# Kernel tuning notes

Measured on AMD Instinct MI355X. Metric: run time of the kernel, lower is better.

Reference implementation:

```python
import jax, jax.numpy as jnp
import numpy as np

B, NH, WH, WW, C, NPOS = 64, 16, 16, 16, 64, 288
N = WH * WW


def setup_inputs() -> dict:
    key = jax.random.key(0)
    k1, k2, k3 = jax.random.split(key, 3)
    query = jax.random.normal(k1, (B, NH, N, C), dtype=jnp.float32)
    attn_logits = jax.random.normal(k2, (B, NH, N, N), dtype=jnp.float32)
    pos_emb = jax.random.normal(k3, (C, NPOS), dtype=jnp.float32) * 0.02
    return {"query": query, "attn_logits": attn_logits, "pos_emb": pos_emb,
            "Wh": WH, "Ww": WW, "npos_max": NPOS}


def _rev_cumsum(x):
    # flip -> cumsum -> flip along last axis
    return jnp.flip(jnp.cumsum(jnp.flip(x, -1), axis=-1), -1)


def reference(query, attn_logits, pos_emb, Wh, Ww, npos_max):
    B_, nH, N_, C_ = query.shape
    gates = jax.nn.sigmoid(attn_logits)                       # (B,nH,N,N)
    gates_h = gates.swapaxes(-1, -2).reshape(B_, nH, N_, Ww, Wh)
    gates_w = gates.reshape(B_, nH, N_, Wh, Ww)
    pos_h = _rev_cumsum(gates_h).reshape(B_, nH, N_, N_).swapaxes(-1, -2)
    pos_w = _rev_cumsum(gates_w).reshape(B_, nH, N_, N_)
    pos = pos_h * Ww + pos_w
    pos = jnp.minimum(pos, npos_max - 1)
    pos_floor = jnp.floor(pos)
    pos_ceil_i = jnp.ceil(pos).astype(jnp.int32)
    pos_floor_i = pos_floor.astype(jnp.int32)
    # (B,nH,N,C) @ (C,npos) -> (B,nH,N,npos)
    logits_int = jnp.einsum('bhnc,cp->bhnp', query, pos_emb)
    logits_ceil = jnp.take_along_axis(logits_int, pos_ceil_i, axis=-1)
    logits_floor = jnp.take_along_axis(logits_int, pos_floor_i, axis=-1)
    w = pos - pos_floor
    return logits_ceil * w + logits_floor * (1.0 - w)
```

## Files before the change

### kernel.cpp

```cpp
#include <hip/hip_runtime.h>


#define NPOS 288
#define NT   18
#define LTSF 292

typedef __attribute__((ext_vector_type(8))) short bf16x8;
typedef __attribute__((ext_vector_type(4))) float f32x4;

__device__ __forceinline__ unsigned short f2bf(float f) {
    unsigned u = __float_as_uint(f);
    u += 0x7FFF + ((u >> 16) & 1);
    return (unsigned short)(u >> 16);
}
__device__ __forceinline__ unsigned cvt_pk_bf16(float lo, float hi) {
    unsigned r;
    asm("v_cvt_pk_bf16_f32 %0, %1, %2" : "=v"(r) : "v"(lo), "v"(hi));
    return r;
}
__device__ __forceinline__ float fast_exp2(float x) {
    float r;
    asm("v_exp_f32 %0, %1" : "=v"(r) : "v"(x));
    return r;
}
__device__ __forceinline__ float fast_fract(float x) {
    float r;
    asm("v_fract_f32 %0, %1" : "=v"(r) : "v"(x));
    return r;
}

template <int D>
__device__ __forceinline__ float suffix_step(float v) {
    int s = __builtin_amdgcn_update_dpp(0, __float_as_int(v), 0x100 | D, 0xF, 0xF, true);
    return v + __int_as_float(s);
}

__global__ void prep_kernel(const float* __restrict__ pos_emb,
                            short* __restrict__ wsb) {
    int idx = blockIdx.x * blockDim.x + threadIdx.x;
    if (idx >= NT * 2 * 64) return;
    int l = idx & 63;
    int s = (idx >> 6) & 1;
    int t = idx >> 7;
    int col = t * 16 + (l & 15);
    int k0  = s * 32 + (l >> 4) * 8;
    short* dst = wsb + idx * 8;
    #pragma unroll
    for (int j = 0; j < 8; ++j)
        dst[j] = (short)f2bf(pos_emb[(k0 + j) * NPOS + col]);
}

__global__ __launch_bounds__(256, 4) void cope2d_kernel(
    const float* __restrict__ query,
    const float* __restrict__ attn_logits,
    const bf16x8* __restrict__ wsb8,
    float* __restrict__ out)
{
    __shared__ float Lf[2][16 * LTSF];

    const int tid  = threadIdx.x;
    const int lane = tid & 63;
    const int wave = tid >> 6;
    const int blk  = blockIdx.x;
    const int bh   = blk >> 2;
    const int p0   = (blk & 3) * 4;

    int rowbase = bh * 256 + p0 * 16;
    int gb      = rowbase * 256;

    bf16x8 Bf[5][2];
    #pragma unroll
    for (int u = 0; u < 5; ++u) {
        int t = wave + 4 * u;
        if (t < NT) {
            Bf[u][0] = wsb8[(t * 2 + 0) * 64 + lane];
            Bf[u][1] = wsb8[(t * 2 + 1) * 64 + lane];
        }
    }

    const float* qp = query + rowbase * 64 + (lane & 15) * 64 + (lane >> 4) * 8;
    f32x4 q00 = *(const f32x4*)(qp);
    f32x4 q01 = *(const f32x4*)(qp + 4);
    f32x4 q10 = *(const f32x4*)(qp + 32);
    f32x4 q11 = *(const f32x4*)(qp + 36);
    float gn[16];
    {
        const float* gp = attn_logits + gb + tid;
        #pragma unroll
        for (int i = 0; i < 16; ++i)
            gn[i] = gp[i * 256];
    }

    for (int s = 0; s < 4; ++s) {
        union { bf16x8 v; unsigned u[4]; } A0, A1;
        A0.u[0] = cvt_pk_bf16(q00[0], q00[1]);
        A0.u[1] = cvt_pk_bf16(q00[2], q00[3]);
        A0.u[2] = cvt_pk_bf16(q01[0], q01[1]);
        A0.u[3] = cvt_pk_bf16(q01[2], q01[3]);
        A1.u[0] = cvt_pk_bf16(q10[0], q10[1]);
        A1.u[1] = cvt_pk_bf16(q10[2], q10[3]);
        A1.u[2] = cvt_pk_bf16(q11[0], q11[1]);
        A1.u[3] = cvt_pk_bf16(q11[2], q11[3]);

        float* Lfs = Lf[s & 1];
        #pragma unroll
        for (int u = 0; u < 5; ++u) {
            int t = wave + 4 * u;
            if (t < NT) {
                f32x4 c = {0.f, 0.f, 0.f, 0.f};
                c = __builtin_amdgcn_mfma_f32_16x16x32_bf16(A0.v, Bf[u][0], c, 0, 0, 0);
                c = __builtin_amdgcn_mfma_f32_16x16x32_bf16(A1.v, Bf[u][1], c, 0, 0, 0);
                const int col = t * 16 + (lane & 15);
                const int r0  = (lane >> 4) * 4;
                #pragma unroll
                for (int r = 0; r < 4; ++r)
                    Lfs[(r0 + r) * LTSF + col] = c[r];
            }
        }

        float g[16];
        #pragma unroll
        for (int i = 0; i < 16; ++i) {
            float e = fast_exp2(gn[i] * -1.44269504088896f);
            g[i] = __builtin_amdgcn_rcpf(1.0f + e);
        }

        const int gout = gb;

        asm volatile("s_waitcnt lgkmcnt(0)" ::: "memory");
        __builtin_amdgcn_s_barrier();

        if (s < 3) {
            rowbase += 16;
            gb += 16 * 256;
            const float* qp2 = query + rowbase * 64 + (lane & 15) * 64 + (lane >> 4) * 8;
            q00 = *(const f32x4*)(qp2);
            q01 = *(const f32x4*)(qp2 + 4);
            q10 = *(const f32x4*)(qp2 + 32);
            q11 = *(const f32x4*)(qp2 + 36);
            const float* gp2 = attn_logits + gb + tid;
            #pragma unroll
            for (int i = 0; i < 16; ++i)
                gn[i] = gp2[i * 256];
        }

        float* op = out + gout + tid;
        float run = 0.f;
        #pragma unroll
        for (int half = 1; half >= 0; --half) {
            const int i0 = half * 8;
            float r8[8];
            #pragma unroll
            for (int k = 7; k >= 0; --k) { run += g[i0 + k]; r8[k] = run; }

            float w8[8]; int fi8[8];
            #pragma unroll
            for (int k = 0; k < 8; ++k) {
                float pw = suffix_step<8>(suffix_step<4>(suffix_step<2>(suffix_step<1>(g[i0 + k]))));
                float pos = r8[k] * 16.0f + pw;
                fi8[k] = (int)pos;
                w8[k]  = fast_fract(pos);
            }
            float lf8[8], lc8[8];
            #pragma unroll
            for (int k = 0; k < 8; ++k) {
                const float* Lr = Lfs + (i0 + k) * LTSF;
                lf8[k] = Lr[fi8[k]];
                lc8[k] = Lr[fi8[k] + 1];
            }
            #pragma unroll
            for (int k = 0; k < 8; ++k)
                op[(i0 + k) * 256] = lf8[k] + w8[k] * (lc8[k] - lf8[k]);
        }
    }
}

extern "C" void kernel_launch(void* const* d_in, const int* in_sizes, int n_in,
                              void* d_out, int out_size, void* d_ws, size_t ws_size,
                              hipStream_t stream) {
    const float* query       = (const float*)d_in[0];
    const float* attn_logits = (const float*)d_in[1];
    const float* pos_emb     = (const float*)d_in[2];
    float* outp = (float*)d_out;
    short* wsb  = (short*)d_ws;

    prep_kernel<<<9, 256, 0, stream>>>(pos_emb, wsb);
    cope2d_kernel<<<4096, 256, 0, stream>>>(query, attn_logits,
                                            (const bf16x8*)d_ws, outp);
}
```

Measured before the change: 122.0 us.

## Vectorize gate loads and stores with cross-wave suffix sums via LDS

Each thread now handles four consecutive columns of four rows instead of one column of sixteen rows, so attn_logits loads and output stores become 16-byte vectors. The row-wise suffix sum across waves is done by writing per-wave partial column sums to a new LDS buffer. The in-row suffix sum is done locally plus masked DPP row shifts. Stores are marked nontemporal, and launch bounds drop from 4 to 3 blocks per SM to make room for the extra registers and LDS. The trade-off is extra LDS traffic, a serial loop over the other waves' partial sums, and lower occupancy.

```diff
diff --git a/kernel.cpp b/kernel.cpp
--- a/kernel.cpp
+++ b/kernel.cpp
@@ -19,20 +19,18 @@
     return r;
 }
 __device__ __forceinline__ float fast_exp2(float x) {
-    float r;
-    asm("v_exp_f32 %0, %1" : "=v"(r) : "v"(x));
-    return r;
+    float r; asm("v_exp_f32 %0, %1" : "=v"(r) : "v"(x)); return r;
 }
 __device__ __forceinline__ float fast_fract(float x) {
-    float r;
-    asm("v_fract_f32 %0, %1" : "=v"(r) : "v"(x));
-    return r;
-}
-
+    float r; asm("v_fract_f32 %0, %1" : "=v"(r) : "v"(x)); return r;
+}
+__device__ __forceinline__ float sigmoid_f(float x) {
+    return __builtin_amdgcn_rcpf(1.0f + fast_exp2(x * -1.44269504088896f));
+}
 template <int D>
-__device__ __forceinline__ float suffix_step(float v) {
+__device__ __forceinline__ float row_shl(float v) {
     int s = __builtin_amdgcn_update_dpp(0, __float_as_int(v), 0x100 | D, 0xF, 0xF, true);
-    return v + __int_as_float(s);
+    return __int_as_float(s);
 }
 
 __global__ void prep_kernel(const float* __restrict__ pos_emb,
@@ -50,13 +48,14 @@
         dst[j] = (short)f2bf(pos_emb[(k0 + j) * NPOS + col]);
 }
 
-__global__ __launch_bounds__(256, 4) void cope2d_kernel(
+__global__ __launch_bounds__(256, 3) void cope2d_kernel(
     const float* __restrict__ query,
     const float* __restrict__ attn_logits,
     const bf16x8* __restrict__ wsb8,
     float* __restrict__ out)
 {
     __shared__ float Lf[2][16 * LTSF];
+    __shared__ float Bs[2][4 * 256];
 
     const int tid  = threadIdx.x;
     const int lane = tid & 63;
@@ -67,6 +66,11 @@
 
     int rowbase = bh * 256 + p0 * 16;
     int gb      = rowbase * 256;
+
+    const int l3 = lane & 3;
+    const float m1 = (l3 < 3) ? 1.0f : 0.0f;
+    const float m2 = (l3 < 2) ? 1.0f : 0.0f;
+    const float m3 = (l3 < 1) ? 1.0f : 0.0f;
 
     bf16x8 Bf[5][2];
     #pragma unroll
@@ -83,12 +87,12 @@
     f32x4 q01 = *(const f32x4*)(qp + 4);
     f32x4 q10 = *(const f32x4*)(qp + 32);
     f32x4 q11 = *(const f32x4*)(qp + 36);
-    float gn[16];
+    f32x4 gnv[4];
     {
-        const float* gp = attn_logits + gb + tid;
-        #pragma unroll
-        for (int i = 0; i < 16; ++i)
-            gn[i] = gp[i * 256];
+        const float* gp = attn_logits + gb + wave * 4 * 256 + lane * 4;
+        #pragma unroll
+        for (int j = 0; j < 4; ++j)
+            gnv[j] = *(const f32x4*)(gp + j * 256);
     }
 
     for (int s = 0; s < 4; ++s) {
@@ -118,17 +122,25 @@
             }
         }
 
-        float g[16];
-        #pragma unroll
-        for (int i = 0; i < 16; ++i) {
-            float e = fast_exp2(gn[i] * -1.44269504088896f);
-            g[i] = __builtin_amdgcn_rcpf(1.0f + e);
+        f32x4 gs[4];
+        #pragma unroll
+        for (int j = 0; j < 4; ++j)
+            #pragma unroll
+            for (int c4 = 0; c4 < 4; ++c4)
+                gs[j][c4] = sigmoid_f(gnv[j][c4]);
+        {
+            f32x4 bsv = gs[0] + gs[1] + gs[2] + gs[3];
+            *(f32x4*)&Bs[s & 1][wave * 256 + lane * 4] = bsv;
         }
 
         const int gout = gb;
 
         asm volatile("s_waitcnt lgkmcnt(0)" ::: "memory");
         __builtin_amdgcn_s_barrier();
+
+        f32x4 SA = {0.f, 0.f, 0.f, 0.f};
+        for (int w2 = wave + 1; w2 < 4; ++w2)
+            SA += *(const f32x4*)&Bs[s & 1][w2 * 256 + lane * 4];
 
         if (s < 3) {
             rowbase += 16;
@@ -138,39 +150,42 @@
             q01 = *(const f32x4*)(qp2 + 4);
             q10 = *(const f32x4*)(qp2 + 32);
             q11 = *(const f32x4*)(qp2 + 36);
-            const float* gp2 = attn_logits + gb + tid;
+            const float* gp2 = attn_logits + gb + wave * 4 * 256 + lane * 4;
             #pragma unroll
-            for (int i = 0; i < 16; ++i)
-                gn[i] = gp2[i * 256];
-        }
-
-        float* op = out + gout + tid;
-        float run = 0.f;
-        #pragma unroll
-        for (int half = 1; half >= 0; --half) {
-            const int i0 = half * 8;
-            float r8[8];
-            #pragma unroll
-            for (int k = 7; k >= 0; --k) { run += g[i0 + k]; r8[k] = run; }
-
-            float w8[8]; int fi8[8];
-            #pragma unroll
-            for (int k = 0; k < 8; ++k) {
-                float pw = suffix_step<8>(suffix_step<4>(suffix_step<2>(suffix_step<1>(g[i0 + k]))));
-                float pos = r8[k] * 16.0f + pw;
-                fi8[k] = (int)pos;
-                w8[k]  = fast_fract(pos);
-            }
-            float lf8[8], lc8[8];
-            #pragma unroll
-            for (int k = 0; k < 8; ++k) {
-                const float* Lr = Lfs + (i0 + k) * LTSF;
-                lf8[k] = Lr[fi8[k]];
-                lc8[k] = Lr[fi8[k] + 1];
-            }
-            #pragma unroll
-            for (int k = 0; k < 8; ++k)
-                op[(i0 + k) * 256] = lf8[k] + w8[k] * (lc8[k] - lf8[k]);
+            for (int j = 0; j < 4; ++j)
+                gnv[j] = *(const f32x4*)(gp2 + j * 256);
+        }
+
+        float a0 = SA[0], a1 = SA[1], a2 = SA[2], a3 = SA[3];
+        float* op = out + gout + (wave * 4) * 256 + lane * 4;
+        #pragma unroll
+        for (int j = 3; j >= 0; --j) {
+            float g0 = gs[j][0], g1 = gs[j][1], g2 = gs[j][2], g3 = gs[j][3];
+            float s3 = g3, s2 = g2 + g3, s1 = g1 + s2, s0 = g0 + s1;
+            float R = fmaf(m1, row_shl<1>(s0),
+                      fmaf(m2, row_shl<2>(s0), m3 * row_shl<3>(s0)));
+            a0 += g0; a1 += g1; a2 += g2; a3 += g3;
+
+            float pos0 = fmaf(a0, 16.0f, s0 + R);
+            float pos1 = fmaf(a1, 16.0f, s1 + R);
+            float pos2 = fmaf(a2, 16.0f, s2 + R);
+            float pos3 = fmaf(a3, 16.0f, s3 + R);
+            int  fi0 = (int)pos0, fi1 = (int)pos1, fi2 = (int)pos2, fi3 = (int)pos3;
+            float w0 = fast_fract(pos0), w1 = fast_fract(pos1);
+            float w2 = fast_fract(pos2), w3 = fast_fract(pos3);
+
+            const float* Lr = Lfs + (wave * 4 + j) * LTSF;
+            float lf0 = Lr[fi0], lc0 = Lr[fi0 + 1];
+            float lf1 = Lr[fi1], lc1 = Lr[fi1 + 1];
+            float lf2 = Lr[fi2], lc2 = Lr[fi2 + 1];
+            float lf3 = Lr[fi3], lc3 = Lr[fi3 + 1];
+
+            f32x4 o;
+            o[0] = lf0 + w0 * (lc0 - lf0);
+            o[1] = lf1 + w1 * (lc1 - lf1);
+            o[2] = lf2 + w2 * (lc2 - lf2);
+            o[3] = lf3 + w3 * (lc3 - lf3);
+            __builtin_nontemporal_store(o, (f32x4*)(op + j * 256));
         }
     }
 }
```

Measured after the change: 119.0 us. -2.4%, faster.
